# Performance work log

Measured on AMD Instinct MI355X. Metric: run time of the kernel, lower is better.

The kernel has to match this reference:

```python
import jax, jax.numpy as jnp
import numpy as np

NHEAD = 4
DIM = 256

def rotate_half(x):
    # interleaved: out[..., ::2] = -x[..., 1::2]; out[..., 1::2] = x[..., ::2]
    xe = x[..., ::2]
    xo = x[..., 1::2]
    return jnp.stack([-xo, xe], axis=-1).reshape(x.shape)

def rope_2d(q, k, H, W):
    Dh = q.shape[-1]
    half = Dh // 2
    inv_freq = 1.0 / (10000.0 ** (jnp.arange(half, dtype=jnp.float32) / half))  # [half]
    yy, xx = jnp.meshgrid(jnp.arange(H, dtype=jnp.float32), jnp.arange(W, dtype=jnp.float32), indexing='ij')
    ang_y = yy.reshape(-1)[:, None] * inv_freq  # [N, half]
    ang_x = xx.reshape(-1)[:, None] * inv_freq  # [N, half]
    cy, sy = jnp.cos(ang_y), jnp.sin(ang_y)
    cx, sx = jnp.cos(ang_x), jnp.sin(ang_x)
    def rot(t):
        t1 = t[..., :half]          # y-rotated half
        t2 = t[..., half:2 * half]  # x-rotated half
        ty = t1 * cy + rotate_half(t1) * sy
        tx = t2 * cx + rotate_half(t2) * sx
        return jnp.concatenate([ty, tx, t[..., 2 * half:]], axis=-1)
    return rot(q), rot(k)

def layernorm(x, g, b, eps=1e-5):
    mu = jnp.mean(x, axis=-1, keepdims=True)
    var = jnp.var(x, axis=-1, keepdims=True)
    return (x - mu) / jnp.sqrt(var + eps) * g + b

def setup_inputs() -> dict:
    key = jax.random.key(0)
    ks = jax.random.split(key, 8)
    B, Hs, Ws, C = 4, 48, 48, DIM
    N = Hs * Ws
    s = 0.02
    return {
        'x': jax.random.normal(ks[0], (B, N, C), dtype=jnp.float32),
        'Wqkv': jax.random.normal(ks[1], (3 * C, C), dtype=jnp.float32) * s,
        'Wproj': jax.random.normal(ks[2], (C, C), dtype=jnp.float32) * s,
        'g1': jnp.ones((C,), jnp.float32), 'b1': jnp.zeros((C,), jnp.float32),
        'g2': jnp.ones((C,), jnp.float32), 'b2': jnp.zeros((C,), jnp.float32),
        'W1': jax.random.normal(ks[3], (4 * C, C), dtype=jnp.float32) * s,
        'bf1': jnp.zeros((4 * C,), jnp.float32),
        'W2': jax.random.normal(ks[4], (C, 4 * C), dtype=jnp.float32) * s,
        'bf2': jnp.zeros((C,), jnp.float32),
        'H': Hs, 'W': Ws,
    }

def reference(x, Wqkv, Wproj, g1, b1, g2, b2, W1, bf1, W2, bf2, H, W):
    B, N, C = x.shape
    dh = C // NHEAD
    qkv = (x @ Wqkv.T).reshape(B, N, 3, NHEAD, dh).transpose(2, 0, 3, 1, 4)  # [3,B,h,N,dh]
    q, k, v = qkv[0], qkv[1], qkv[2]
    q, k = rope_2d(q, k, H, W)
    scores = jnp.einsum('bhnd,bhmd->bhnm', q, k) / jnp.sqrt(jnp.float32(dh))
    attn = jax.nn.softmax(scores, axis=-1)  # drop_attn is identity (p=0)
    out = jnp.einsum('bhnm,bhmd->bhnd', attn, v).transpose(0, 2, 1, 3).reshape(B, N, C)
    x = x + out @ Wproj.T
    x = layernorm(x, g1, b1)
    h = jax.nn.gelu(x @ W1.T + bf1, approximate=False)
    x = x + h @ W2.T + bf2
    return layernorm(x, g2, b2)
```

## Files before the change

### kernel.cpp

```cpp
#include <hip/hip_runtime.h>
#include <hip/hip_bf16.h>
#include <math.h>

typedef __hip_bfloat16 bf16;
typedef __attribute__((ext_vector_type(8))) short short8;
typedef __attribute__((ext_vector_type(4))) short short4v;
typedef __attribute__((ext_vector_type(4))) float f32x4;

#define NSEQ 2304
#define CDIM 256
#define NHD  4
#define DH   64

#if __has_builtin(__builtin_amdgcn_exp2f)
#define EXP2F __builtin_amdgcn_exp2f
#else
#define EXP2F exp2f
#endif

static __device__ __forceinline__ f32x4 mfma_bf16(short8 a, short8 b, f32x4 c) {
  return __builtin_amdgcn_mfma_f32_16x16x32_bf16(a, b, c, 0, 0, 0);
}
static __device__ __forceinline__ short8 ld8(const bf16* p) {
  return *reinterpret_cast<const short8*>(p);
}
static __device__ __forceinline__ short8 lds8(const bf16* p) {
  return *reinterpret_cast<const short8*>(p);
}
static __device__ __forceinline__ float b2f(short v) {
  unsigned int u = ((unsigned int)(unsigned short)v) << 16;
  return __uint_as_float(u);
}
static __device__ __forceinline__ short f2b(float f) {
  bf16 h = __float2bfloat16(f);
  return *reinterpret_cast<short*>(&h);
}

__global__ __launch_bounds__(256) void detect_kernel(const void* __restrict__ xraw,
                                                     int* __restrict__ flag) {
  int t = threadIdx.x;
  const unsigned short* s = (const unsigned short*)xraw;
  int bad = 0;
#pragma unroll
  for (int i = 0; i < 8; ++i) {
    unsigned idx = (((unsigned)(t * 8 + i)) * 9173u) & ((1u << 20) - 1);
    unsigned short v = s[idx * 2];
    unsigned e = (v >> 7) & 0xFFu;
    if (e > 133u) bad++;
  }
  __shared__ int tot;
  if (t == 0) tot = 0;
  __syncthreads();
  atomicAdd(&tot, bad);
  __syncthreads();
  if (t == 0) flag[0] = (tot >= 16) ? 1 : 0;
}

__global__ __launch_bounds__(256) void cvt_all_kernel(const void* sx, const void* sqkv, const void* sproj,
                                                      const void* sw1, const void* sw2,
                                                      const void* g1, const void* b1, const void* g2,
                                                      const void* b2, const void* bias1, const void* bias2,
                                                      bf16* dx, bf16* dqkv, bf16* dproj,
                                                      bf16* dw1, bf16* dw2, bf16* dsm,
                                                      const int* __restrict__ flag) {
  int is32 = flag[0];
  int bid = blockIdx.x;
  const void* src; bf16* dst; int i4;
  if (bid < 2304)      { src = sx;    dst = dx;    i4 = bid * 256 + threadIdx.x; }
  else if (bid < 2496) { src = sqkv;  dst = dqkv;  i4 = (bid - 2304) * 256 + threadIdx.x; }
  else if (bid < 2560) { src = sproj; dst = dproj; i4 = (bid - 2496) * 256 + threadIdx.x; }
  else if (bid < 2816) { src = sw1;   dst = dw1;   i4 = (bid - 2560) * 256 + threadIdx.x; }
  else if (bid < 3072) { src = sw2;   dst = dw2;   i4 = (bid - 2816) * 256 + threadIdx.x; }
  else {
    const void* srcs[6] = {g1, b1, g2, b2, bias1, bias2};
    const int ns[6] = {256, 256, 256, 256, 1024, 256};
    const int off[6] = {0, 256, 512, 768, 1024, 2048};
    int t = threadIdx.x;
#pragma unroll
    for (int j = 0; j < 6; ++j)
      for (int i = t; i < ns[j]; i += 256) {
        if (is32) dsm[off[j] + i] = __float2bfloat16(((const float*)srcs[j])[i]);
        else      dsm[off[j] + i] = ((const bf16*)srcs[j])[i];
      }
    return;
  }
  if (is32) {
    float4 v = ((const float4*)src)[i4];
    short4v o;
    o[0] = f2b(v.x); o[1] = f2b(v.y); o[2] = f2b(v.z); o[3] = f2b(v.w);
    ((short4v*)dst)[i4] = o;
  } else {
    ((short4v*)dst)[i4] = ((const short4v*)src)[i4];
  }
}

__global__ __launch_bounds__(256, 1) void qkv_kernel(const bf16* __restrict__ X,
                                                     const bf16* __restrict__ Wqkv,
                                                     bf16* __restrict__ Q, bf16* __restrict__ K,
                                                     bf16* __restrict__ Vt,
                                                     const int* __restrict__ Wp) {
  int wave = threadIdx.x >> 6, lane = threadIdx.x & 63;
  int l15 = lane & 15, quad = lane >> 4;
  int m0 = (blockIdx.x * 4 + wave) * 64;
  int n0 = blockIdx.y * 64;
  const bf16* arow = X + (size_t)(m0 + l15) * CDIM + quad * 8;
  const bf16* brow = Wqkv + (size_t)(n0 + l15) * CDIM + quad * 8;
  f32x4 z = {0.f, 0.f, 0.f, 0.f};
  f32x4 acc[4][4];
#pragma unroll
  for (int j = 0; j < 4; ++j)
#pragma unroll
    for (int i = 0; i < 4; ++i) acc[j][i] = z;

  short8 a[4], b[4];
#pragma unroll
  for (int i = 0; i < 4; ++i) a[i] = ld8(arow + (size_t)i * 16 * CDIM);
#pragma unroll
  for (int j = 0; j < 4; ++j) b[j] = ld8(brow + (size_t)j * 16 * CDIM);
#pragma unroll
  for (int kk = 32; kk <= CDIM; kk += 32) {
    short8 an[4], bn[4];
    if (kk < CDIM) {
#pragma unroll
      for (int i = 0; i < 4; ++i) an[i] = ld8(arow + (size_t)i * 16 * CDIM + kk);
#pragma unroll
      for (int j = 0; j < 4; ++j) bn[j] = ld8(brow + (size_t)j * 16 * CDIM + kk);
    }
#pragma unroll
    for (int j = 0; j < 4; ++j)
#pragma unroll
      for (int i = 0; i < 4; ++i) acc[j][i] = mfma_bf16(b[j], a[i], acc[j][i]);
    if (kk < CDIM) {
#pragma unroll
      for (int i = 0; i < 4; ++i) a[i] = an[i];
#pragma unroll
      for (int j = 0; j < 4; ++j) b[j] = bn[j];
    }
  }

  int which = n0 >> 8, h = (n0 & 255) >> 6;
  if (which == 2) {
#pragma unroll
    for (int j = 0; j < 4; ++j) {
      int d0 = j * 16 + quad * 4;
#pragma unroll
      for (int i = 0; i < 4; ++i) {
        int gm = m0 + i * 16 + l15;
        int bb = gm / NSEQ, n = gm % NSEQ;
        int bh = bb * NHD + h;
#pragma unroll
        for (int r = 0; r < 4; ++r)
          Vt[((size_t)bh * DH + d0 + r) * NSEQ + n] = __float2bfloat16(acc[j][i][r]);
      }
    }
  } else {
    int Wv = Wp[0];
    if (Wv <= 0 || Wv > 65536) Wv = 48;
    bf16* dst = (which == 0) ? Q : K;
    const float cc = -0.28782313662425574f;
    const float EC1 = 0.7498942434f, EC2 = 0.5623413252f, EC3 = 0.4216965034f;
#pragma unroll
    for (int i = 0; i < 4; ++i) {
      int gm = m0 + i * 16 + l15;
      int bb = gm / NSEQ, n = gm % NSEQ;
      int bh = bb * NHD + h;
      int py = n / Wv, px = n - py * Wv;
#pragma unroll
      for (int j = 0; j < 4; ++j) {
        int d0 = j * 16 + quad * 4;
        float pos = (d0 & 32) ? (float)px : (float)py;
        int base = d0 & 31;
        float fb = __expf(cc * (float)base);
        float f0 = fb, f1 = fb * EC1, f2 = fb * EC2, f3 = fb * EC3;
        float s0, c0, s1, c1, s2, c2, s3, c3;
        __sincosf(pos * f0, &s0, &c0);
        __sincosf(pos * f1, &s1, &c1);
        __sincosf(pos * f2, &s2, &c2);
        __sincosf(pos * f3, &s3, &c3);
        float a0 = acc[j][i][0], a1 = acc[j][i][1], a2 = acc[j][i][2], a3 = acc[j][i][3];
        short4v ov;
        ov[0] = f2b(a0 * c0 - a1 * s0);
        ov[1] = f2b(a1 * c1 + a0 * s1);
        ov[2] = f2b(a2 * c2 - a3 * s2);
        ov[3] = f2b(a3 * c3 + a2 * s3);
        *reinterpret_cast<short4v*>(dst + ((size_t)bh * NSEQ + n) * DH + d0) = ov;
      }
    }
  }
}

__global__ __launch_bounds__(256) void attn_kernel(const bf16* __restrict__ Q, const bf16* __restrict__ K,
                                                   const bf16* __restrict__ Vt, bf16* __restrict__ AO) {
  int bh = blockIdx.x, qt = blockIdx.y;
  int tid = threadIdx.x;
  int wave = tid >> 6, lane = tid & 63;
  int l15 = lane & 15, quad = lane >> 4;
  int m0 = qt * 64 + wave * 16;
  const bf16* Qb = Q + (size_t)bh * NSEQ * DH;
  const bf16* Kb = K + (size_t)bh * NSEQ * DH;
  const bf16* Vb = Vt + (size_t)bh * DH * NSEQ;

  __shared__ __align__(16) bf16 kbuf[2][64 * 72];
  __shared__ __align__(16) bf16 vbuf[2][64 * 72];
  __shared__ __align__(16) bf16 plds[4][16 * 72];

  int i1 = tid, i2 = tid + 256;
  int r1 = i1 >> 3, s1 = (i1 & 7) * 8;
  int r2 = i2 >> 3, s2 = (i2 & 7) * 8;

  const float QS = 0.18033688011112042f;
  short8 bq0 = ld8(Qb + (size_t)(m0 + l15) * DH + quad * 8);
  short8 bq1 = ld8(Qb + (size_t)(m0 + l15) * DH + 32 + quad * 8);
#pragma unroll
  for (int i = 0; i < 8; ++i) {
    bq0[i] = f2b(b2f(bq0[i]) * QS);
    bq1[i] = f2b(b2f(bq1[i]) * QS);
  }

  f32x4 z = {0.f, 0.f, 0.f, 0.f};
  f32x4 o[4] = {z, z, z, z};
  float l_run = 0.f;
  bf16* pb = plds[wave];

  {
    short8 ka = ld8(Kb + (size_t)r1 * DH + s1);
    short8 kb2 = ld8(Kb + (size_t)r2 * DH + s2);
    short8 va = ld8(Vb + (size_t)r1 * NSEQ + s1);
    short8 vb2 = ld8(Vb + (size_t)r2 * NSEQ + s2);
    *reinterpret_cast<short8*>(kbuf[0] + r1 * 72 + s1) = ka;
    *reinterpret_cast<short8*>(kbuf[0] + r2 * 72 + s2) = kb2;
    *reinterpret_cast<short8*>(vbuf[0] + r1 * 72 + s1) = va;
    *reinterpret_cast<short8*>(vbuf[0] + r2 * 72 + s2) = vb2;
  }
  __syncthreads();

  for (int it = 0; it < NSEQ / 64; ++it) {
    int cur = it & 1;
    bool more = (it + 1 < NSEQ / 64);
    short8 ka, kb2, va, vb2;
    if (more) {
      int kc = (it + 1) * 64;
      ka  = ld8(Kb + (size_t)(kc + r1) * DH + s1);
      kb2 = ld8(Kb + (size_t)(kc + r2) * DH + s2);
      va  = ld8(Vb + (size_t)r1 * NSEQ + kc + s1);
      vb2 = ld8(Vb + (size_t)r2 * NSEQ + kc + s2);
    }

    const bf16* kb = kbuf[cur];
    const bf16* vb = vbuf[cur];

    f32x4 s[4];
#pragma unroll
    for (int kt = 0; kt < 4; ++kt) {
      const bf16* kp = kb + (size_t)(kt * 16 + l15) * 72 + quad * 8;
      s[kt] = mfma_bf16(lds8(kp), bq0, z);
      s[kt] = mfma_bf16(lds8(kp + 32), bq1, s[kt]);
    }

    float ls = 0.f;
#pragma unroll
    for (int kt = 0; kt < 4; ++kt) {
      float p0 = EXP2F(s[kt][0]);
      float p1 = EXP2F(s[kt][1]);
      float p2 = EXP2F(s[kt][2]);
      float p3 = EXP2F(s[kt][3]);
      ls += (p0 + p1) + (p2 + p3);
      short4v pk;
      pk[0] = f2b(p0); pk[1] = f2b(p1); pk[2] = f2b(p2); pk[3] = f2b(p3);
      *reinterpret_cast<short4v*>(pb + l15 * 72 + kt * 16 + quad * 4) = pk;
    }
    l_run += ls;

#pragma unroll
    for (int kt2 = 0; kt2 < 2; ++kt2) {
      short8 pfrag = lds8(pb + l15 * 72 + kt2 * 32 + quad * 8);
#pragma unroll
      for (int t = 0; t < 4; ++t) {
        short8 av = lds8(vb + (size_t)(t * 16 + l15) * 72 + kt2 * 32 + quad * 8);
        o[t] = mfma_bf16(av, pfrag, o[t]);
      }
    }

    if (more) {
      bf16* kn = kbuf[1 - cur];
      bf16* vn = vbuf[1 - cur];
      *reinterpret_cast<short8*>(kn + r1 * 72 + s1) = ka;
      *reinterpret_cast<short8*>(kn + r2 * 72 + s2) = kb2;
      *reinterpret_cast<short8*>(vn + r1 * 72 + s1) = va;
      *reinterpret_cast<short8*>(vn + r2 * 72 + s2) = vb2;
    }
    __syncthreads();
  }

  l_run += __shfl_xor(l_run, 16);
  l_run += __shfl_xor(l_run, 32);
  float inv = 1.f / l_run;
  int b = bh >> 2, h = bh & 3;
  bf16* orow = AO + ((size_t)b * NSEQ + (m0 + l15)) * CDIM + h * DH;
#pragma unroll
  for (int t = 0; t < 4; ++t) {
    short4v ov;
#pragma unroll
    for (int r = 0; r < 4; ++r) ov[r] = f2b(o[t][r] * inv);
    *reinterpret_cast<short4v*>(orow + t * 16 + quad * 4) = ov;
  }
}

template <int KD, int EPI, int TI>
__global__ __launch_bounds__(256) void gemm128(const bf16* __restrict__ A, const bf16* __restrict__ Wm,
                                               const bf16* __restrict__ bias, const bf16* __restrict__ res,
                                               bf16* __restrict__ outp, int NC) {
  constexpr int KS = KD / 32;
  constexpr int AR = TI * 32;
  int tid = threadIdx.x;
  int wave = tid >> 6, lane = tid & 63;
  int l15 = lane & 15, quad = lane >> 4;
  int wm = (wave >> 1) * (TI * 16);
  int wn = (wave & 1) * 64;
  int m0 = blockIdx.x * AR;
  int n0 = blockIdx.y * 128;

  __shared__ __align__(16) bf16 abuf[2][AR * 40];
  __shared__ __align__(16) bf16 bbuf[2][128 * 40];

  int sr = tid >> 2, sc = (tid & 3) * 8;

  const bf16* ag[TI / 2];
#pragma unroll
  for (int u = 0; u < TI / 2; ++u) ag[u] = A + (size_t)(m0 + sr + u * 64) * KD + sc;
  const bf16* bg0 = Wm + (size_t)(n0 + sr) * KD + sc;
  const bf16* bg1 = Wm + (size_t)(n0 + 64 + sr) * KD + sc;

  f32x4 z = {0.f, 0.f, 0.f, 0.f};
  f32x4 acc[4][TI];
#pragma unroll
  for (int j = 0; j < 4; ++j)
#pragma unroll
    for (int i = 0; i < TI; ++i) acc[j][i] = z;

#pragma unroll
  for (int u = 0; u < TI / 2; ++u)
    *reinterpret_cast<short8*>(abuf[0] + (sr + u * 64) * 40 + sc) = ld8(ag[u]);
  *reinterpret_cast<short8*>(bbuf[0] + sr * 40 + sc) = ld8(bg0);
  *reinterpret_cast<short8*>(bbuf[0] + (64 + sr) * 40 + sc) = ld8(bg1);
  __syncthreads();

  for (int s = 0; s < KS; ++s) {
    int cur = s & 1;
    bool more = (s + 1 < KS);
    short8 anx[TI / 2], bnx0, bnx1;
    if (more) {
#pragma unroll
      for (int u = 0; u < TI / 2; ++u) anx[u] = ld8(ag[u] + (s + 1) * 32);
      bnx0 = ld8(bg0 + (s + 1) * 32);
      bnx1 = ld8(bg1 + (s + 1) * 32);
    }
    short8 af[TI], bf_[4];
#pragma unroll
    for (int i = 0; i < TI; ++i)
      af[i] = lds8(abuf[cur] + (size_t)(wm + i * 16 + l15) * 40 + quad * 8);
#pragma unroll
    for (int j = 0; j < 4; ++j)
      bf_[j] = lds8(bbuf[cur] + (size_t)(wn + j * 16 + l15) * 40 + quad * 8);
#pragma unroll
    for (int j = 0; j < 4; ++j)
#pragma unroll
      for (int i = 0; i < TI; ++i)
        acc[j][i] = mfma_bf16(bf_[j], af[i], acc[j][i]);
    if (more) {
#pragma unroll
      for (int u = 0; u < TI / 2; ++u)
        *reinterpret_cast<short8*>(abuf[1 - cur] + (sr + u * 64) * 40 + sc) = anx[u];
      *reinterpret_cast<short8*>(bbuf[1 - cur] + sr * 40 + sc) = bnx0;
      *reinterpret_cast<short8*>(bbuf[1 - cur] + (64 + sr) * 40 + sc) = bnx1;
    }
    __syncthreads();
  }

#pragma unroll
  for (int j = 0; j < 4; ++j) {
    int col0 = n0 + wn + j * 16 + quad * 4;
    float bb4[4];
    if (EPI != 0) {
      short4v bl = *reinterpret_cast<const short4v*>(bias + col0);
#pragma unroll
      for (int r = 0; r < 4; ++r) bb4[r] = b2f(bl[r]);
    }
#pragma unroll
    for (int i = 0; i < TI; ++i) {
      size_t idx = (size_t)(m0 + wm + i * 16 + l15) * NC + col0;
      short4v ov;
      if (EPI == 0) {
        short4v rl = *reinterpret_cast<const short4v*>(res + idx);
#pragma unroll
        for (int r = 0; r < 4; ++r) ov[r] = f2b(acc[j][i][r] + b2f(rl[r]));
      } else if (EPI == 1) {
#pragma unroll
        for (int r = 0; r < 4; ++r) {
          float hv = acc[j][i][r] + bb4[r];
          ov[r] = f2b(0.5f * hv * (1.f + erff(hv * 0.70710678118f)));
        }
      } else {
        short4v rl = *reinterpret_cast<const short4v*>(res + idx);
#pragma unroll
        for (int r = 0; r < 4; ++r) ov[r] = f2b(acc[j][i][r] + bb4[r] + b2f(rl[r]));
      }
      *reinterpret_cast<short4v*>(outp + idx) = ov;
    }
  }
}

__global__ __launch_bounds__(256) void ln_kernel(const bf16* __restrict__ X, const bf16* __restrict__ g,
                                                 const bf16* __restrict__ bv, bf16* __restrict__ out) {
  int row = blockIdx.x * 4 + (threadIdx.x >> 6);
  int lane = threadIdx.x & 63;
  short4v raw = *reinterpret_cast<const short4v*>(X + (size_t)row * CDIM + lane * 4);
  float vv[4];
  float s = 0.f, sq = 0.f;
#pragma unroll
  for (int i = 0; i < 4; ++i) {
    float f = b2f(raw[i]);
    vv[i] = f; s += f; sq += f * f;
  }
#pragma unroll
  for (int off = 1; off < 64; off <<= 1) { s += __shfl_xor(s, off); sq += __shfl_xor(sq, off); }
  float mu = s * (1.f / CDIM);
  float var = sq * (1.f / CDIM) - mu * mu;
  float rstd = rsqrtf(var + 1e-5f);
#pragma unroll
  for (int i = 0; i < 4; ++i) {
    int c = lane * 4 + i;
    out[(size_t)row * CDIM + c] =
        __float2bfloat16((vv[i] - mu) * rstd * __bfloat162float(g[c]) + __bfloat162float(bv[c]));
  }
}

__global__ __launch_bounds__(256) void ln_out_kernel(const bf16* __restrict__ X, const bf16* __restrict__ g,
                                                     const bf16* __restrict__ bv, void* __restrict__ out,
                                                     const int* __restrict__ flag) {
  int is32 = flag[0];
  int row = blockIdx.x * 4 + (threadIdx.x >> 6);
  int lane = threadIdx.x & 63;
  short4v raw = *reinterpret_cast<const short4v*>(X + (size_t)row * CDIM + lane * 4);
  float vv[4];
  float s = 0.f, sq = 0.f;
#pragma unroll
  for (int i = 0; i < 4; ++i) {
    float f = b2f(raw[i]);
    vv[i] = f; s += f; sq += f * f;
  }
#pragma unroll
  for (int off = 1; off < 64; off <<= 1) { s += __shfl_xor(s, off); sq += __shfl_xor(sq, off); }
  float mu = s * (1.f / CDIM);
  float var = sq * (1.f / CDIM) - mu * mu;
  float rstd = rsqrtf(var + 1e-5f);
#pragma unroll
  for (int i = 0; i < 4; ++i) {
    int c = lane * 4 + i;
    size_t idx = (size_t)row * CDIM + c;
    float v = (vv[i] - mu) * rstd * __bfloat162float(g[c]) + __bfloat162float(bv[c]);
    if (is32) ((float*)out)[idx] = v;
    else      ((bf16*)out)[idx] = __float2bfloat16(v);
  }
}

extern "C" void kernel_launch(void* const* d_in, const int* in_sizes, int n_in,
                              void* d_out, int out_size, void* d_ws, size_t ws_size,
                              hipStream_t stream) {
  const int* Wp = (const int*)d_in[12];

  char* ws = (char*)d_ws;
  const size_t SZ = 4718592;
  bf16* Qc  = (bf16*)(ws + 0 * SZ);
  bf16* Kc  = (bf16*)(ws + 1 * SZ);
  bf16* Vt  = (bf16*)(ws + 2 * SZ);
  bf16* AO  = (bf16*)(ws + 3 * SZ);
  bf16* F   = (bf16*)(ws + 4 * SZ);
  bf16* Y   = (bf16*)(ws + 5 * SZ);
  bf16* xc  = (bf16*)(ws + 6 * SZ);
  bf16* G   = (bf16*)(ws + 0);
  bf16* Wqkvc  = (bf16*)(ws + 7 * SZ);
  bf16* Wprojc = (bf16*)(ws + 7 * SZ + 393216);
  bf16* W1c    = (bf16*)(ws + 7 * SZ + 524288);
  bf16* W2c    = (bf16*)(ws + 7 * SZ + 1048576);
  bf16* smallc = (bf16*)(ws + 7 * SZ + 1572864);
  bf16* g1c  = smallc + 0;
  bf16* b1c  = smallc + 256;
  bf16* g2c  = smallc + 512;
  bf16* b2c  = smallc + 768;
  bf16* bf1c = smallc + 1024;
  bf16* bf2c = smallc + 2048;
  int*  flagp = (int*)(ws + 7 * SZ + 1581568);
  bf16* outsc = (bf16*)d_out;

  detect_kernel<<<1, 256, 0, stream>>>(d_in[0], flagp);
  cvt_all_kernel<<<3073, 256, 0, stream>>>(d_in[0], d_in[1], d_in[2], d_in[7], d_in[9],
                                           d_in[3], d_in[4], d_in[5], d_in[6], d_in[8], d_in[10],
                                           xc, Wqkvc, Wprojc, W1c, W2c, smallc, flagp);

  qkv_kernel<<<dim3(36, 12), 256, 0, stream>>>(xc, Wqkvc, Qc, Kc, Vt, Wp);
  attn_kernel<<<dim3(16, 36), 256, 0, stream>>>(Qc, Kc, Vt, AO);
  gemm128<256, 0, 2><<<dim3(144, 2), 256, 0, stream>>>(AO, Wprojc, nullptr, xc, outsc, 256);
  ln_kernel<<<2304, 256, 0, stream>>>(outsc, g1c, b1c, F);
  gemm128<256, 1, 4><<<dim3(72, 8), 256, 0, stream>>>(F, W1c, bf1c, nullptr, G, 1024);
  gemm128<1024, 2, 2><<<dim3(144, 2), 256, 0, stream>>>(G, W2c, bf2c, F, Y, 256);
  ln_out_kernel<<<2304, 256, 0, stream>>>(Y, g2c, b2c, d_out, flagp);
}
```

Measured before the change: 219.1 us.

## Shrink attention blocks to 3 waves and load V fragments directly from global

The attention kernel now uses 192-thread blocks (three 16-row query waves, 48 rows per block) across a 16x48 grid instead of 256 threads and 64 rows. V tiles are no longer staged through shared memory; each wave loads its V MFMA operands straight from global memory into registers every iteration, and only K is double-buffered in LDS. This cuts LDS use and the V staging traffic to allow more resident blocks, but each wave now fetches V separately, raising global/L2 traffic and register pressure, and V loads are exposed with no prefetch.

```diff
diff --git a/kernel.cpp b/kernel.cpp
--- a/kernel.cpp
+++ b/kernel.cpp
@@ -189,24 +189,25 @@
   }
 }
 
-__global__ __launch_bounds__(256) void attn_kernel(const bf16* __restrict__ Q, const bf16* __restrict__ K,
-                                                   const bf16* __restrict__ Vt, bf16* __restrict__ AO) {
+__global__ __launch_bounds__(192, 3) void attn_kernel(const bf16* __restrict__ Q, const bf16* __restrict__ K,
+                                                      const bf16* __restrict__ Vt, bf16* __restrict__ AO) {
   int bh = blockIdx.x, qt = blockIdx.y;
   int tid = threadIdx.x;
   int wave = tid >> 6, lane = tid & 63;
   int l15 = lane & 15, quad = lane >> 4;
-  int m0 = qt * 64 + wave * 16;
+  int m0 = qt * 48 + wave * 16;
   const bf16* Qb = Q + (size_t)bh * NSEQ * DH;
   const bf16* Kb = K + (size_t)bh * NSEQ * DH;
   const bf16* Vb = Vt + (size_t)bh * DH * NSEQ;
 
   __shared__ __align__(16) bf16 kbuf[2][64 * 72];
-  __shared__ __align__(16) bf16 vbuf[2][64 * 72];
-  __shared__ __align__(16) bf16 plds[4][16 * 72];
-
-  int i1 = tid, i2 = tid + 256;
-  int r1 = i1 >> 3, s1 = (i1 & 7) * 8;
-  int r2 = i2 >> 3, s2 = (i2 & 7) * 8;
+  __shared__ __align__(16) bf16 plds[3][16 * 72];
+
+  int sa = tid, sb = tid + 192, sc = tid + 384;
+  int ra = sa >> 3, ca = (sa & 7) * 8;
+  int rb = sb >> 3, cb = (sb & 7) * 8;
+  int rc = sc >> 3, cc2 = (sc & 7) * 8;
+  bool third = (tid < 128);
 
   const float QS = 0.18033688011112042f;
   short8 bq0 = ld8(Qb + (size_t)(m0 + l15) * DH + quad * 8);
@@ -221,33 +222,35 @@
   f32x4 o[4] = {z, z, z, z};
   float l_run = 0.f;
   bf16* pb = plds[wave];
-
-  {
-    short8 ka = ld8(Kb + (size_t)r1 * DH + s1);
-    short8 kb2 = ld8(Kb + (size_t)r2 * DH + s2);
-    short8 va = ld8(Vb + (size_t)r1 * NSEQ + s1);
-    short8 vb2 = ld8(Vb + (size_t)r2 * NSEQ + s2);
-    *reinterpret_cast<short8*>(kbuf[0] + r1 * 72 + s1) = ka;
-    *reinterpret_cast<short8*>(kbuf[0] + r2 * 72 + s2) = kb2;
-    *reinterpret_cast<short8*>(vbuf[0] + r1 * 72 + s1) = va;
-    *reinterpret_cast<short8*>(vbuf[0] + r2 * 72 + s2) = vb2;
-  }
+  const bf16* vrow = Vb + (size_t)l15 * NSEQ + quad * 8;
+
+  *reinterpret_cast<short8*>(kbuf[0] + ra * 72 + ca) = ld8(Kb + (size_t)ra * DH + ca);
+  *reinterpret_cast<short8*>(kbuf[0] + rb * 72 + cb) = ld8(Kb + (size_t)rb * DH + cb);
+  if (third)
+    *reinterpret_cast<short8*>(kbuf[0] + rc * 72 + cc2) = ld8(Kb + (size_t)rc * DH + cc2);
   __syncthreads();
 
   for (int it = 0; it < NSEQ / 64; ++it) {
     int cur = it & 1;
     bool more = (it + 1 < NSEQ / 64);
-    short8 ka, kb2, va, vb2;
+    int kc = it * 64;
+
+    short8 ka, kb2, kc3;
     if (more) {
-      int kc = (it + 1) * 64;
-      ka  = ld8(Kb + (size_t)(kc + r1) * DH + s1);
-      kb2 = ld8(Kb + (size_t)(kc + r2) * DH + s2);
-      va  = ld8(Vb + (size_t)r1 * NSEQ + kc + s1);
-      vb2 = ld8(Vb + (size_t)r2 * NSEQ + kc + s2);
-    }
+      int kn = kc + 64;
+      ka  = ld8(Kb + (size_t)(kn + ra) * DH + ca);
+      kb2 = ld8(Kb + (size_t)(kn + rb) * DH + cb);
+      if (third) kc3 = ld8(Kb + (size_t)(kn + rc) * DH + cc2);
+    }
+
+    short8 vf[8];
+#pragma unroll
+    for (int kt2 = 0; kt2 < 2; ++kt2)
+#pragma unroll
+      for (int t = 0; t < 4; ++t)
+        vf[kt2 * 4 + t] = ld8(vrow + (size_t)t * 16 * NSEQ + kc + kt2 * 32);
 
     const bf16* kb = kbuf[cur];
-    const bf16* vb = vbuf[cur];
 
     f32x4 s[4];
 #pragma unroll
@@ -275,19 +278,15 @@
     for (int kt2 = 0; kt2 < 2; ++kt2) {
       short8 pfrag = lds8(pb + l15 * 72 + kt2 * 32 + quad * 8);
 #pragma unroll
-      for (int t = 0; t < 4; ++t) {
-        short8 av = lds8(vb + (size_t)(t * 16 + l15) * 72 + kt2 * 32 + quad * 8);
-        o[t] = mfma_bf16(av, pfrag, o[t]);
-      }
+      for (int t = 0; t < 4; ++t)
+        o[t] = mfma_bf16(vf[kt2 * 4 + t], pfrag, o[t]);
     }
 
     if (more) {
-      bf16* kn = kbuf[1 - cur];
-      bf16* vn = vbuf[1 - cur];
-      *reinterpret_cast<short8*>(kn + r1 * 72 + s1) = ka;
-      *reinterpret_cast<short8*>(kn + r2 * 72 + s2) = kb2;
-      *reinterpret_cast<short8*>(vn + r1 * 72 + s1) = va;
-      *reinterpret_cast<short8*>(vn + r2 * 72 + s2) = vb2;
+      bf16* kn_ = kbuf[1 - cur];
+      *reinterpret_cast<short8*>(kn_ + ra * 72 + ca) = ka;
+      *reinterpret_cast<short8*>(kn_ + rb * 72 + cb) = kb2;
+      if (third) *reinterpret_cast<short8*>(kn_ + rc * 72 + cc2) = kc3;
     }
     __syncthreads();
   }
@@ -499,7 +498,7 @@
                                            xc, Wqkvc, Wprojc, W1c, W2c, smallc, flagp);
 
   qkv_kernel<<<dim3(36, 12), 256, 0, stream>>>(xc, Wqkvc, Qc, Kc, Vt, Wp);
-  attn_kernel<<<dim3(16, 36), 256, 0, stream>>>(Qc, Kc, Vt, AO);
+  attn_kernel<<<dim3(16, 48), 192, 0, stream>>>(Qc, Kc, Vt, AO);
   gemm128<256, 0, 2><<<dim3(144, 2), 256, 0, stream>>>(AO, Wprojc, nullptr, xc, outsc, 256);
   ln_kernel<<<2304, 256, 0, stream>>>(outsc, g1c, b1c, F);
   gemm128<256, 1, 4><<<dim3(72, 8), 256, 0, stream>>>(F, W1c, bf1c, nullptr, G, 1024);
```

After: 249.8 us. 14.0% more time.

## Process two query tiles per wave in attention to reuse K/V fragments

Applied to the files above, without the earlier changes.

The attention block shrinks from four waves to two, and each wave now handles 32 query rows instead of 16. Each K and V fragment read from LDS feeds two MFMAs, which halves LDS reads per unit of compute. Each thread now loads four K/V chunks per tile instead of two. In exchange there are fewer waves per block and more registers per thread, which may lower occupancy and latency hiding; grid size is unchanged.

```diff
diff --git a/kernel.cpp b/kernel.cpp
--- a/kernel.cpp
+++ b/kernel.cpp
@@ -189,75 +189,85 @@
   }
 }
 
-__global__ __launch_bounds__(256) void attn_kernel(const bf16* __restrict__ Q, const bf16* __restrict__ K,
-                                                   const bf16* __restrict__ Vt, bf16* __restrict__ AO) {
+__global__ __launch_bounds__(128, 2) void attn_kernel(const bf16* __restrict__ Q, const bf16* __restrict__ K,
+                                                      const bf16* __restrict__ Vt, bf16* __restrict__ AO) {
   int bh = blockIdx.x, qt = blockIdx.y;
   int tid = threadIdx.x;
   int wave = tid >> 6, lane = tid & 63;
   int l15 = lane & 15, quad = lane >> 4;
-  int m0 = qt * 64 + wave * 16;
+  int m0 = qt * 64 + wave * 32;
   const bf16* Qb = Q + (size_t)bh * NSEQ * DH;
   const bf16* Kb = K + (size_t)bh * NSEQ * DH;
   const bf16* Vb = Vt + (size_t)bh * DH * NSEQ;
 
   __shared__ __align__(16) bf16 kbuf[2][64 * 72];
   __shared__ __align__(16) bf16 vbuf[2][64 * 72];
-  __shared__ __align__(16) bf16 plds[4][16 * 72];
-
-  int i1 = tid, i2 = tid + 256;
-  int r1 = i1 >> 3, s1 = (i1 & 7) * 8;
-  int r2 = i2 >> 3, s2 = (i2 & 7) * 8;
+  __shared__ __align__(16) bf16 plds[2][32 * 72];
+
+  int rs[4], cs[4];
+#pragma unroll
+  for (int j = 0; j < 4; ++j) {
+    int i = tid + j * 128;
+    rs[j] = i >> 3;
+    cs[j] = (i & 7) * 8;
+  }
 
   const float QS = 0.18033688011112042f;
-  short8 bq0 = ld8(Qb + (size_t)(m0 + l15) * DH + quad * 8);
-  short8 bq1 = ld8(Qb + (size_t)(m0 + l15) * DH + 32 + quad * 8);
+  short8 qa0 = ld8(Qb + (size_t)(m0 + l15) * DH + quad * 8);
+  short8 qa1 = ld8(Qb + (size_t)(m0 + l15) * DH + 32 + quad * 8);
+  short8 qb0 = ld8(Qb + (size_t)(m0 + 16 + l15) * DH + quad * 8);
+  short8 qb1 = ld8(Qb + (size_t)(m0 + 16 + l15) * DH + 32 + quad * 8);
 #pragma unroll
   for (int i = 0; i < 8; ++i) {
-    bq0[i] = f2b(b2f(bq0[i]) * QS);
-    bq1[i] = f2b(b2f(bq1[i]) * QS);
+    qa0[i] = f2b(b2f(qa0[i]) * QS);
+    qa1[i] = f2b(b2f(qa1[i]) * QS);
+    qb0[i] = f2b(b2f(qb0[i]) * QS);
+    qb1[i] = f2b(b2f(qb1[i]) * QS);
   }
 
   f32x4 z = {0.f, 0.f, 0.f, 0.f};
   f32x4 o[4] = {z, z, z, z};
-  float l_run = 0.f;
+  f32x4 o2[4] = {z, z, z, z};
+  float l_run = 0.f, l_run2 = 0.f;
   bf16* pb = plds[wave];
 
-  {
-    short8 ka = ld8(Kb + (size_t)r1 * DH + s1);
-    short8 kb2 = ld8(Kb + (size_t)r2 * DH + s2);
-    short8 va = ld8(Vb + (size_t)r1 * NSEQ + s1);
-    short8 vb2 = ld8(Vb + (size_t)r2 * NSEQ + s2);
-    *reinterpret_cast<short8*>(kbuf[0] + r1 * 72 + s1) = ka;
-    *reinterpret_cast<short8*>(kbuf[0] + r2 * 72 + s2) = kb2;
-    *reinterpret_cast<short8*>(vbuf[0] + r1 * 72 + s1) = va;
-    *reinterpret_cast<short8*>(vbuf[0] + r2 * 72 + s2) = vb2;
+#pragma unroll
+  for (int j = 0; j < 4; ++j) {
+    *reinterpret_cast<short8*>(kbuf[0] + rs[j] * 72 + cs[j]) = ld8(Kb + (size_t)rs[j] * DH + cs[j]);
+    *reinterpret_cast<short8*>(vbuf[0] + rs[j] * 72 + cs[j]) = ld8(Vb + (size_t)rs[j] * NSEQ + cs[j]);
   }
   __syncthreads();
 
   for (int it = 0; it < NSEQ / 64; ++it) {
     int cur = it & 1;
     bool more = (it + 1 < NSEQ / 64);
-    short8 ka, kb2, va, vb2;
+
+    short8 kpre[4], vpre[4];
     if (more) {
-      int kc = (it + 1) * 64;
-      ka  = ld8(Kb + (size_t)(kc + r1) * DH + s1);
-      kb2 = ld8(Kb + (size_t)(kc + r2) * DH + s2);
-      va  = ld8(Vb + (size_t)r1 * NSEQ + kc + s1);
-      vb2 = ld8(Vb + (size_t)r2 * NSEQ + kc + s2);
+      int kn = (it + 1) * 64;
+#pragma unroll
+      for (int j = 0; j < 4; ++j) {
+        kpre[j] = ld8(Kb + (size_t)(kn + rs[j]) * DH + cs[j]);
+        vpre[j] = ld8(Vb + (size_t)rs[j] * NSEQ + kn + cs[j]);
+      }
     }
 
     const bf16* kb = kbuf[cur];
     const bf16* vb = vbuf[cur];
 
-    f32x4 s[4];
+    f32x4 s[4], s2[4];
 #pragma unroll
     for (int kt = 0; kt < 4; ++kt) {
       const bf16* kp = kb + (size_t)(kt * 16 + l15) * 72 + quad * 8;
-      s[kt] = mfma_bf16(lds8(kp), bq0, z);
-      s[kt] = mfma_bf16(lds8(kp + 32), bq1, s[kt]);
-    }
-
-    float ls = 0.f;
+      short8 kf0 = lds8(kp);
+      short8 kf1 = lds8(kp + 32);
+      s[kt] = mfma_bf16(kf0, qa0, z);
+      s[kt] = mfma_bf16(kf1, qa1, s[kt]);
+      s2[kt] = mfma_bf16(kf0, qb0, z);
+      s2[kt] = mfma_bf16(kf1, qb1, s2[kt]);
+    }
+
+    float ls = 0.f, ls2 = 0.f;
 #pragma unroll
     for (int kt = 0; kt < 4; ++kt) {
       float p0 = EXP2F(s[kt][0]);
@@ -268,41 +278,61 @@
       short4v pk;
       pk[0] = f2b(p0); pk[1] = f2b(p1); pk[2] = f2b(p2); pk[3] = f2b(p3);
       *reinterpret_cast<short4v*>(pb + l15 * 72 + kt * 16 + quad * 4) = pk;
+      float q0 = EXP2F(s2[kt][0]);
+      float q1 = EXP2F(s2[kt][1]);
+      float q2 = EXP2F(s2[kt][2]);
+      float q3 = EXP2F(s2[kt][3]);
+      ls2 += (q0 + q1) + (q2 + q3);
+      short4v pk2;
+      pk2[0] = f2b(q0); pk2[1] = f2b(q1); pk2[2] = f2b(q2); pk2[3] = f2b(q3);
+      *reinterpret_cast<short4v*>(pb + (16 + l15) * 72 + kt * 16 + quad * 4) = pk2;
     }
     l_run += ls;
+    l_run2 += ls2;
 
 #pragma unroll
     for (int kt2 = 0; kt2 < 2; ++kt2) {
-      short8 pfrag = lds8(pb + l15 * 72 + kt2 * 32 + quad * 8);
+      short8 pfA = lds8(pb + l15 * 72 + kt2 * 32 + quad * 8);
+      short8 pfB = lds8(pb + (16 + l15) * 72 + kt2 * 32 + quad * 8);
 #pragma unroll
       for (int t = 0; t < 4; ++t) {
-        short8 av = lds8(vb + (size_t)(t * 16 + l15) * 72 + kt2 * 32 + quad * 8);
-        o[t] = mfma_bf16(av, pfrag, o[t]);
+        short8 vf = lds8(vb + (size_t)(t * 16 + l15) * 72 + kt2 * 32 + quad * 8);
+        o[t] = mfma_bf16(vf, pfA, o[t]);
+        o2[t] = mfma_bf16(vf, pfB, o2[t]);
       }
     }
 
     if (more) {
-      bf16* kn = kbuf[1 - cur];
-      bf16* vn = vbuf[1 - cur];
-      *reinterpret_cast<short8*>(kn + r1 * 72 + s1) = ka;
-      *reinterpret_cast<short8*>(kn + r2 * 72 + s2) = kb2;
-      *reinterpret_cast<short8*>(vn + r1 * 72 + s1) = va;
-      *reinterpret_cast<short8*>(vn + r2 * 72 + s2) = vb2;
+      bf16* kn_ = kbuf[1 - cur];
+      bf16* vn_ = vbuf[1 - cur];
+#pragma unroll
+      for (int j = 0; j < 4; ++j) {
+        *reinterpret_cast<short8*>(kn_ + rs[j] * 72 + cs[j]) = kpre[j];
+        *reinterpret_cast<short8*>(vn_ + rs[j] * 72 + cs[j]) = vpre[j];
+      }
     }
     __syncthreads();
   }
 
   l_run += __shfl_xor(l_run, 16);
   l_run += __shfl_xor(l_run, 32);
+  l_run2 += __shfl_xor(l_run2, 16);
+  l_run2 += __shfl_xor(l_run2, 32);
   float inv = 1.f / l_run;
+  float inv2 = 1.f / l_run2;
   int b = bh >> 2, h = bh & 3;
   bf16* orow = AO + ((size_t)b * NSEQ + (m0 + l15)) * CDIM + h * DH;
+  bf16* orow2 = AO + ((size_t)b * NSEQ + (m0 + 16 + l15)) * CDIM + h * DH;
 #pragma unroll
   for (int t = 0; t < 4; ++t) {
-    short4v ov;
-#pragma unroll
-    for (int r = 0; r < 4; ++r) ov[r] = f2b(o[t][r] * inv);
+    short4v ov, ov2;
+#pragma unroll
+    for (int r = 0; r < 4; ++r) {
+      ov[r] = f2b(o[t][r] * inv);
+      ov2[r] = f2b(o2[t][r] * inv2);
+    }
     *reinterpret_cast<short4v*>(orow + t * 16 + quad * 4) = ov;
+    *reinterpret_cast<short4v*>(orow2 + t * 16 + quad * 4) = ov2;
   }
 }
 
@@ -499,7 +529,7 @@
                                            xc, Wqkvc, Wprojc, W1c, W2c, smallc, flagp);
 
   qkv_kernel<<<dim3(36, 12), 256, 0, stream>>>(xc, Wqkvc, Qc, Kc, Vt, Wp);
-  attn_kernel<<<dim3(16, 36), 256, 0, stream>>>(Qc, Kc, Vt, AO);
+  attn_kernel<<<dim3(16, 36), 128, 0, stream>>>(Qc, Kc, Vt, AO);
   gemm128<256, 0, 2><<<dim3(144, 2), 256, 0, stream>>>(AO, Wprojc, nullptr, xc, outsc, 256);
   ln_kernel<<<2304, 256, 0, stream>>>(outsc, g1c, b1c, F);
   gemm128<256, 1, 4><<<dim3(72, 8), 256, 0, stream>>>(F, W1c, bf1c, nullptr, G, 1024);
```

New measurement: 217.7 us. Within noise of the previous version (-0.6%).
